# Performance work log

Measured on AMD Instinct MI355X. Metric: run time of the kernel, lower is better.

The kernel has to match this reference:

```python
import jax, jax.numpy as jnp
import numpy as np

P, Q, D = 16, 16, 1  # AR order, MA order, differencing order (init_kwargs)
S0 = 1048577         # raw series length -> 2**20 after d=1 differencing


def setup_inputs() -> dict:
    key = jax.random.key(0)
    k1, k2, k3 = jax.random.split(key, 3)
    series = jax.random.normal(k1, (1, S0, 1), dtype=jnp.float32)
    # nn.Linear(p,1,bias=False).weight flattened to (p,), applied to y[t-p:t] in order
    w_ar = jax.random.normal(k2, (P,), dtype=jnp.float32) * 0.1
    w_ma = jax.random.normal(k3, (Q,), dtype=jnp.float32) * 0.1
    return {"series": series, "w_ar": w_ar, "w_ma": w_ma}


def reference(series, w_ar, w_ma):
    # difference(): d-th order differencing (B=1, C=1 -> work on flat vector)
    y = series[0, :, 0]
    for _ in range(D):
        y = y[1:] - y[:-1]
    S = y.shape[0]
    m = max(P, Q)

    # AR windows: windows[t] = y[t-P:t] (zero-padded at front; only read when t > m >= P)
    ypad = jnp.concatenate([jnp.zeros((P,), y.dtype), y])
    windows = jnp.stack([ypad[k:k + S] for k in range(P)], axis=-1)  # (S, P)

    t_idx = jnp.arange(S)

    def step(e_hist, inp):
        # e_hist: last Q errors, oldest first (matches e_list[t-q:t] ordering)
        y_t, win, t = inp
        ar = jnp.dot(win, w_ar)
        ma = jnp.dot(e_hist, w_ma)
        pred = jnp.where(t > m, ar + ma, jnp.zeros((), y.dtype))
        err = y_t - pred
        e_hist = jnp.concatenate([e_hist[1:], err[None]])
        return e_hist, err

    e0 = jnp.zeros((Q,), y.dtype)
    _, errs = jax.lax.scan(step, e0, (y, windows, t_idx))
    # mse_loss: mean of squared one-step errors
    return jnp.mean(errs ** 2)
```

## Files before the change

kernel.cpp:

```cpp
#include <hip/hip_runtime.h>


#define S_TOTAL 1048576
#define WCHUNK  256
#define NBLK    1024
#define WLOOK   192
#define WTILE   448
#define RUN     7
#define SER     468
#define GUARD   64
#define BUFW    (GUARD + SER + 4)
#define POISON  0xAAAAAAAAu
#define NSUB    32
#define SUBSTRIDE 16

__device__ __forceinline__ void wbar() { __builtin_amdgcn_wave_barrier(); }

__device__ __forceinline__ void square17(float (&cc)[17])
{
    float b[17];
    #pragma unroll
    for (int m = 0; m <= 16; ++m) {
        float s = 0.0f;
        #pragma unroll
        for (int i = 0; i <= 16; ++i) {
            int j = 2 * m - i;
            if (j >= 0 && j <= 16) {
                float t = cc[i] * cc[j];
                s = (i & 1) ? s - t : s + t;
            }
        }
        b[m] = s;
    }
    #pragma unroll
    for (int m = 0; m <= 16; ++m) cc[m] = b[m];
}

template <int LOG_S>
__device__ __forceinline__ void stageW(const float* in, float* out,
                                       const float (&cc)[17], int lane)
{
    constexpr int S = 1 << LOG_S;
    wbar();
    const int ob = (lane & (S - 1)) + RUN * S * (lane >> LOG_S);
    float x[16 + RUN];
    #pragma unroll
    for (int m = 0; m < 16 + RUN; ++m)
        x[m] = in[GUARD + ob + S * (m - 16)];
    #pragma unroll
    for (int i = 0; i < RUN; ++i) {
        float acc = x[16 + i];
        #pragma unroll
        for (int j = 1; j <= 16; ++j) {
            float v = x[16 + i - j];
            acc = (j & 1) ? fmaf(-cc[j], v, acc)
                          : fmaf(cc[j], v, acc);
        }
        out[GUARD + ob + S * i] = acc;
    }
    wbar();
}

__global__ __launch_bounds__(256, 4) void k_arima(const float* __restrict__ series,
                                                  const float* __restrict__ w_ar,
                                                  const float* __restrict__ w_ma,
                                                  float* __restrict__ partials,
                                                  float* __restrict__ out)
{
    __shared__ __align__(16) float buf[8][BUFW];
    __shared__ float redLDS[4];
    __shared__ int lastFlag;

    const int tid  = threadIdx.x;
    const int w    = tid >> 6;
    const int lane = tid & 63;

    float* bufA = buf[2 * w];
    float* bufB = buf[2 * w + 1];

    const int wbase = (blockIdx.x * 4 + w) * WCHUNK;
    const int T0    = wbase - WLOOK;
    const int gbase = T0 - 16;

    bufA[lane] = 0.0f;
    bufB[lane] = 0.0f;

    if (gbase >= 0 && gbase + SER <= S_TOTAL + 1) {
        const float4* gp = (const float4*)(series + gbase);
        float4* lp = (float4*)(bufA + GUARD);
        lp[lane] = gp[lane];
        if (lane < SER / 4 - 64) lp[64 + lane] = gp[64 + lane];
    } else {
        for (int i = lane; i < SER; i += 64) {
            int g = gbase + i;
            g = min(max(g, 0), S_TOTAL);
            bufA[GUARD + i] = series[g];
        }
    }

    float cc[17];
    cc[0] = 1.0f;
    #pragma unroll
    for (int m = 1; m <= 16; ++m) cc[m] = w_ma[16 - m];

    wbar();

    {
        const int o0 = RUN * lane;
        float s[17 + RUN], y[16 + RUN];
        #pragma unroll
        for (int m = 0; m < 17 + RUN; ++m) s[m] = bufA[GUARD + o0 + m];
        #pragma unroll
        for (int m = 0; m < 16 + RUN; ++m) y[m] = s[m + 1] - s[m];
        #pragma unroll
        for (int i = 0; i < RUN; ++i) {
            float acc = y[16 + i];
            #pragma unroll
            for (int j = 1; j <= 16; ++j)
                acc = fmaf(-w_ar[16 - j], y[16 + i - j], acc);
            if (T0 < 17) {
                int t = T0 + o0 + i;
                if (t <= 16) {
                    acc = 0.0f;
                    if (t >= 1) {
                        acc = y[16 + i];
                        for (int j = 1; j < t; ++j)
                            acc += w_ma[16 - j] * y[16 + i - j];
                    }
                }
            }
            bufB[GUARD + o0 + i] = acc;
        }
    }

    stageW<0>(bufB, bufA, cc, lane);  square17(cc);
    stageW<1>(bufA, bufB, cc, lane);  square17(cc);
    stageW<2>(bufB, bufA, cc, lane);  square17(cc);

    float acc = 0.0f;
    {
        const int rr   = lane & 7;
        const int g    = lane >> 3;
        const int base = GUARD + WLOOK - 72 + rr + 32 * g;
        float h[16];
        #pragma unroll
        for (int j = 0; j < 16; ++j) h[j] = 0.0f;
        #pragma unroll
        for (int s = 0; s < 13; ++s) {
            float e = bufA[base + 8 * s];
            #pragma unroll
            for (int j = 0; j < 16; ++j) e = fmaf(-cc[j + 1], h[j], e);
            #pragma unroll
            for (int j = 15; j >= 1; --j) h[j] = h[j - 1];
            h[0] = e;
            if (s >= 9) acc += e * e;
        }
    }

    #pragma unroll
    for (int off = 32; off > 0; off >>= 1)
        acc += __shfl_down(acc, off, 64);
    if (lane == 0) redLDS[w] = acc;
    __syncthreads();

    if (tid == 0) {
        float tot = redLDS[0] + redLDS[1] + redLDS[2] + redLDS[3];
        int last = 0;
        if (partials) {
            unsigned* tick = (unsigned*)(partials + NBLK);
            (void)atomicExch(&partials[blockIdx.x], tot);
            asm volatile("s_waitcnt vmcnt(0)" ::: "memory");
            unsigned so = atomicAdd(&tick[(blockIdx.x >> 5) * SUBSTRIDE], 1u);
            if (((so - POISON - 31u) & 31u) == 0u) {
                unsigned mo = atomicAdd(&tick[NSUB * SUBSTRIDE], 1u);
                last = ((mo - POISON - 31u) & 31u) == 0u;
            }
        } else {
            if (blockIdx.x == 0) {
                float y0 = series[1] - series[0];
                tot += y0 * y0;
            }
            atomicAdd(out, tot * (1.0f / (float)S_TOTAL));
        }
        lastFlag = last;
    }
    __syncthreads();

    if (lastFlag) {
        float s = 0.0f;
        #pragma unroll
        for (int i = 0; i < NBLK / 256; ++i)
            s += atomicAdd(&partials[tid * (NBLK / 256) + i], 0.0f);
        #pragma unroll
        for (int off = 32; off > 0; off >>= 1)
            s += __shfl_down(s, off, 64);
        if (lane == 0) redLDS[w] = s;
        __syncthreads();
        if (tid == 0) {
            float y0 = series[1] - series[0];
            float tot = redLDS[0] + redLDS[1] + redLDS[2] + redLDS[3] + y0 * y0;
            out[0] = tot * (1.0f / (float)S_TOTAL);
        }
    }
}

extern "C" void kernel_launch(void* const* d_in, const int* in_sizes, int n_in,
                              void* d_out, int out_size, void* d_ws, size_t ws_size,
                              hipStream_t stream) {
    const float* series = (const float*)d_in[0];
    const float* w_ar   = (const float*)d_in[1];
    const float* w_ma   = (const float*)d_in[2];
    float* out = (float*)d_out;

    float* partials = nullptr;
    if (d_ws && ws_size >= (NBLK + NSUB * SUBSTRIDE + SUBSTRIDE) * sizeof(float))
        partials = (float*)d_ws;

    k_arima<<<NBLK, 256, 0, stream>>>(series, w_ar, w_ma, partials, out);
}
```

Before: 68.16 us.

## Use skewed LDS layout with float4 accesses and RUN of 8 per lane

Raises the per-lane run length from 7 to 8 and the lookback window from 192 to 256, so each lane's contiguous span is aligned to 4 and can be read and written as float4. A skew function pads the LDS by 4 floats every 32 elements to cut bank conflicts on strided accesses. The trade is more redundant warm-up work per wave from the larger lookback, plus extra index arithmetic. The final recursion start point still uses WLOOK-72, so it stays tied to the new lookback.

```diff
diff --git a/kernel.cpp b/kernel.cpp
--- a/kernel.cpp
+++ b/kernel.cpp
@@ -4,17 +4,19 @@
 #define S_TOTAL 1048576
 #define WCHUNK  256
 #define NBLK    1024
-#define WLOOK   192
-#define WTILE   448
-#define RUN     7
-#define SER     468
+#define WLOOK   256
+#define WTILE   512
+#define RUN     8
+#define SER     532
 #define GUARD   64
-#define BUFW    (GUARD + SER + 4)
+#define BUFW    672
 #define POISON  0xAAAAAAAAu
 #define NSUB    32
 #define SUBSTRIDE 16
 
 __device__ __forceinline__ void wbar() { __builtin_amdgcn_wave_barrier(); }
+
+__device__ __forceinline__ int SKEW(int t) { return t + 4 * (t >> 5); }
 
 __device__ __forceinline__ void square17(float (&cc)[17])
 {
@@ -44,9 +46,18 @@
     wbar();
     const int ob = (lane & (S - 1)) + RUN * S * (lane >> LOG_S);
     float x[16 + RUN];
-    #pragma unroll
-    for (int m = 0; m < 16 + RUN; ++m)
-        x[m] = in[GUARD + ob + S * (m - 16)];
+    if constexpr (LOG_S == 0) {
+        #pragma unroll
+        for (int c = 0; c < 6; ++c) {
+            float4 v = *(const float4*)(in + SKEW(GUARD + ob - 16 + 4 * c));
+            x[4*c+0] = v.x; x[4*c+1] = v.y; x[4*c+2] = v.z; x[4*c+3] = v.w;
+        }
+    } else {
+        #pragma unroll
+        for (int m = 0; m < 16 + RUN; ++m)
+            x[m] = in[SKEW(GUARD + ob + S * (m - 16))];
+    }
+    float o[RUN];
     #pragma unroll
     for (int i = 0; i < RUN; ++i) {
         float acc = x[16 + i];
@@ -56,7 +67,15 @@
             acc = (j & 1) ? fmaf(-cc[j], v, acc)
                           : fmaf(cc[j], v, acc);
         }
-        out[GUARD + ob + S * i] = acc;
+        o[i] = acc;
+    }
+    if constexpr (LOG_S == 0) {
+        *(float4*)(out + SKEW(GUARD + ob))     = make_float4(o[0],o[1],o[2],o[3]);
+        *(float4*)(out + SKEW(GUARD + ob + 4)) = make_float4(o[4],o[5],o[6],o[7]);
+    } else {
+        #pragma unroll
+        for (int i = 0; i < RUN; ++i)
+            out[SKEW(GUARD + ob + S * i)] = o[i];
     }
     wbar();
 }
@@ -82,19 +101,21 @@
     const int T0    = wbase - WLOOK;
     const int gbase = T0 - 16;
 
-    bufA[lane] = 0.0f;
-    bufB[lane] = 0.0f;
+    bufA[SKEW(lane)] = 0.0f;
+    bufB[SKEW(lane)] = 0.0f;
 
     if (gbase >= 0 && gbase + SER <= S_TOTAL + 1) {
         const float4* gp = (const float4*)(series + gbase);
-        float4* lp = (float4*)(bufA + GUARD);
-        lp[lane] = gp[lane];
-        if (lane < SER / 4 - 64) lp[64 + lane] = gp[64 + lane];
+        #pragma unroll
+        for (int c = 0; c < 2; ++c)
+            *(float4*)(bufA + SKEW(GUARD + 4 * (c * 64 + lane))) = gp[c * 64 + lane];
+        if (lane < SER / 4 - 128)
+            *(float4*)(bufA + SKEW(GUARD + 4 * (128 + lane))) = gp[128 + lane];
     } else {
         for (int i = lane; i < SER; i += 64) {
             int g = gbase + i;
             g = min(max(g, 0), S_TOTAL);
-            bufA[GUARD + i] = series[g];
+            bufA[SKEW(GUARD + i)] = series[g];
         }
     }
 
@@ -109,9 +130,14 @@
         const int o0 = RUN * lane;
         float s[17 + RUN], y[16 + RUN];
         #pragma unroll
-        for (int m = 0; m < 17 + RUN; ++m) s[m] = bufA[GUARD + o0 + m];
+        for (int c = 0; c < 6; ++c) {
+            float4 v = *(const float4*)(bufA + SKEW(GUARD + o0 + 4 * c));
+            s[4*c+0] = v.x; s[4*c+1] = v.y; s[4*c+2] = v.z; s[4*c+3] = v.w;
+        }
+        s[24] = bufA[SKEW(GUARD + o0 + 24)];
         #pragma unroll
         for (int m = 0; m < 16 + RUN; ++m) y[m] = s[m + 1] - s[m];
+        float o[RUN];
         #pragma unroll
         for (int i = 0; i < RUN; ++i) {
             float acc = y[16 + i];
@@ -129,8 +155,10 @@
                     }
                 }
             }
-            bufB[GUARD + o0 + i] = acc;
-        }
+            o[i] = acc;
+        }
+        *(float4*)(bufB + SKEW(GUARD + o0))     = make_float4(o[0],o[1],o[2],o[3]);
+        *(float4*)(bufB + SKEW(GUARD + o0 + 4)) = make_float4(o[4],o[5],o[6],o[7]);
     }
 
     stageW<0>(bufB, bufA, cc, lane);  square17(cc);
@@ -147,7 +175,7 @@
         for (int j = 0; j < 16; ++j) h[j] = 0.0f;
         #pragma unroll
         for (int s = 0; s < 13; ++s) {
-            float e = bufA[base + 8 * s];
+            float e = bufA[SKEW(base + 8 * s)];
             #pragma unroll
             for (int j = 0; j < 16; ++j) e = fmaf(-cc[j + 1], h[j], e);
             #pragma unroll
```

Result: no change. 69.46 us (+1.9%).
